# Kernel optimization log

Hardware: AMD Instinct MI355X
Metric: run time of the kernel (lower is better)

Reference implementation:

```python
import jax, jax.numpy as jnp
import numpy as np

EPS = 1e-12  # torch F.normalize eps

def _l2norm(v, axis):
    n = jnp.sqrt(jnp.sum(v * v, axis=axis, keepdims=True))
    return v / jnp.maximum(n, EPS)

def setup_inputs() -> dict:
    key = jax.random.key(0)
    k1, k2 = jax.random.split(key)
    B, N, D, K = 8, 2048, 128, 64
    x = jax.random.normal(k1, (B, N, D), dtype=jnp.float32)
    std1 = 1.0 / np.sqrt(K * D)
    centroids = jax.random.uniform(k2, (K, D), dtype=jnp.float32, minval=-std1, maxval=std1)
    return {"x": x, "centroids": centroids}

def reference(x, centroids):
    # x: [B, N, D], centroids: [K, D]
    B, N, D = x.shape
    K = centroids.shape[0]
    xn = _l2norm(x, axis=-1)                       # descriptor-wise L2 normalize
    res = xn[:, :, None, :] - centroids[None, None]  # [B, N, K, D]
    dist = jnp.sum(res * res, axis=-1)             # [B, N, K] squared distances
    assign = jax.nn.softmax(dist, axis=-1)         # softmax over clusters (NOTE: positive distances, as in source)
    vlad = jnp.einsum('bnk,bnkd->bkd', assign, res)  # weighted residual sum over N
    vlad = _l2norm(vlad, axis=2)                   # intra-normalization per cluster
    vlad = vlad.reshape(B, K * D)
    vlad = _l2norm(vlad, axis=1)                   # global L2 normalize
    return vlad
```

## Files before the change

kernel.cpp:

```cpp
#include <hip/hip_runtime.h>
#include <math.h>

#define BB 8
#define NN 2048
#define DD 128
#define KK 64
#define PP 64
#define NPB (NN / PP)
#define TI 16

__global__ __launch_bounds__(512)
__attribute__((amdgpu_waves_per_eu(4, 4)))
void netvlad_k1(
    const float* __restrict__ x, const float* __restrict__ cent,
    float* __restrict__ part_acc)
{
    const int b    = blockIdx.x >> 6;
    const int p    = blockIdx.x & 63;
    const int t    = threadIdx.x;
    const int h    = t >> 8;
    const int u    = t & 255;
    const int kq   = u >> 3;
    const int pr   = u & 7;
    const int dbase = pr * 16;
    const int wv   = u >> 6;

    __shared__ __align__(16) float xs[2][TI][DD];
    __shared__ __align__(16) float sL[2][TI][4];
    __shared__ __align__(16) float comb[256][36];
    __shared__ float sAc[32][2];

    int off[4];
    #pragma unroll
    for (int jj = 0; jj < 4; ++jj) off[jj] = dbase + (((jj + pr) & 3) << 2);

    const int i0 = u >> 4, tl = u & 15;
    const float* xr = x + ((size_t)b * NN + (size_t)p * NPB + h * TI + i0) * DD;
    float4 v0 = *(const float4*)(xr + tl * 4);
    float4 v1 = *(const float4*)(xr + 64 + tl * 4);

    float4 cA[4], cB[4];
    float cn2a = 0.f, cn2b = 0.f;
    #pragma unroll
    for (int jj = 0; jj < 4; ++jj) {
        cA[jj] = *(const float4*)(cent + (2 * kq) * DD + off[jj]);
        cB[jj] = *(const float4*)(cent + (2 * kq + 1) * DD + off[jj]);
        cn2a += cA[jj].x*cA[jj].x + cA[jj].y*cA[jj].y + cA[jj].z*cA[jj].z + cA[jj].w*cA[jj].w;
        cn2b += cB[jj].x*cB[jj].x + cB[jj].y*cB[jj].y + cB[jj].z*cB[jj].z + cB[jj].w*cB[jj].w;
    }
    #pragma unroll
    for (int m = 1; m < 8; m <<= 1) {
        cn2a += __shfl_xor(cn2a, m);
        cn2b += __shfl_xor(cn2b, m);
    }

    {
        float ss = v0.x*v0.x + v0.y*v0.y + v0.z*v0.z + v0.w*v0.w
                 + v1.x*v1.x + v1.y*v1.y + v1.z*v1.z + v1.w*v1.w;
        #pragma unroll
        for (int m = 1; m < 16; m <<= 1) ss += __shfl_xor(ss, m);
        const float rn = 1.0f / fmaxf(sqrtf(ss), 1e-12f);
        v0.x *= rn; v0.y *= rn; v0.z *= rn; v0.w *= rn;
        v1.x *= rn; v1.y *= rn; v1.z *= rn; v1.w *= rn;
        *(float4*)(&xs[h][i0][tl * 4])      = v0;
        *(float4*)(&xs[h][i0][64 + tl * 4]) = v1;
    }
    __syncthreads();

    float e0[TI], e1[TI];
    #pragma unroll
    for (int i = 0; i < TI; ++i) {
        float S0 = 0.f, S1 = 0.f;
        #pragma unroll
        for (int jj = 0; jj < 4; ++jj) {
            float4 v = *(const float4*)(&xs[h][i][off[jj]]);
            S0 += v.x*cA[jj].x + v.y*cA[jj].y + v.z*cA[jj].z + v.w*cA[jj].w;
            S1 += v.x*cB[jj].x + v.y*cB[jj].y + v.z*cB[jj].z + v.w*cB[jj].w;
        }
        #pragma unroll
        for (int m = 1; m < 8; m <<= 1) {
            S0 += __shfl_xor(S0, m);
            S1 += __shfl_xor(S1, m);
        }
        e0[i] = __expf(cn2a - 2.f * S0);
        e1[i] = __expf(cn2b - 2.f * S1);
        float es = e0[i] + e1[i];
        #pragma unroll
        for (int m = 8; m < 64; m <<= 1) es += __shfl_xor(es, m);
        if ((u & 63) == 0) sL[h][i][wv] = es;
    }
    __syncthreads();

    float4 acc0[4], acc1[4];
    #pragma unroll
    for (int jj = 0; jj < 4; ++jj) {
        acc0[jj] = make_float4(0.f, 0.f, 0.f, 0.f);
        acc1[jj] = make_float4(0.f, 0.f, 0.f, 0.f);
    }
    float sA0 = 0.f, sA1 = 0.f;
    #pragma unroll
    for (int i = 0; i < TI; ++i) {
        const float4 s4 = *(const float4*)(&sL[h][i][0]);
        const float rs = 1.0f / (s4.x + s4.y + s4.z + s4.w);
        const float a0 = e0[i] * rs, a1 = e1[i] * rs;
        sA0 += a0; sA1 += a1;
        #pragma unroll
        for (int jj = 0; jj < 4; ++jj) {
            float4 v = *(const float4*)(&xs[h][i][off[jj]]);
            acc0[jj].x += a0*v.x; acc0[jj].y += a0*v.y; acc0[jj].z += a0*v.z; acc0[jj].w += a0*v.w;
            acc1[jj].x += a1*v.x; acc1[jj].y += a1*v.y; acc1[jj].z += a1*v.z; acc1[jj].w += a1*v.w;
        }
    }

    if (h == 0) {
        #pragma unroll
        for (int jj = 0; jj < 4; ++jj) {
            *(float4*)(&comb[u][jj * 4])      = acc0[jj];
            *(float4*)(&comb[u][16 + jj * 4]) = acc1[jj];
        }
        if (pr == 0) { sAc[kq][0] = sA0; sAc[kq][1] = sA1; }
    }
    __syncthreads();

    if (h == 1) {
        sA0 += sAc[kq][0];
        sA1 += sAc[kq][1];
        const size_t base = (size_t)(b * PP + p) * KK * DD;
        #pragma unroll
        for (int jj = 0; jj < 4; ++jj) {
            const float4 c0 = *(const float4*)(cent + (2 * kq) * DD + off[jj]);
            const float4 c1 = *(const float4*)(cent + (2 * kq + 1) * DD + off[jj]);
            const float4 o0 = *(const float4*)(&comb[u][jj * 4]);
            const float4 o1 = *(const float4*)(&comb[u][16 + jj * 4]);
            float4 r0 = acc0[jj], r1 = acc1[jj];
            r0.x += o0.x; r0.y += o0.y; r0.z += o0.z; r0.w += o0.w;
            r1.x += o1.x; r1.y += o1.y; r1.z += o1.z; r1.w += o1.w;
            r0.x -= sA0 * c0.x; r0.y -= sA0 * c0.y;
            r0.z -= sA0 * c0.z; r0.w -= sA0 * c0.w;
            r1.x -= sA1 * c1.x; r1.y -= sA1 * c1.y;
            r1.z -= sA1 * c1.z; r1.w -= sA1 * c1.w;
            *(float4*)(part_acc + base + (2 * kq) * DD + off[jj])     = r0;
            *(float4*)(part_acc + base + (2 * kq + 1) * DD + off[jj]) = r1;
        }
    }
}

__global__ __launch_bounds__(512) void netvlad_k2(
    const float* __restrict__ part_acc, float* __restrict__ out)
{
    const int b  = blockIdx.x >> 6;
    const int k  = blockIdx.x & 63;
    const int t  = threadIdx.x;
    const int d4 = t & 31;
    const int ps = t >> 5;

    float4 acc = make_float4(0.f, 0.f, 0.f, 0.f);
    const float* base = part_acc + ((size_t)(b * PP) * KK + k) * DD + d4 * 4;
    #pragma unroll
    for (int j = 0; j < 4; ++j) {
        const float4 v = *(const float4*)(base + (size_t)(j * 16 + ps) * KK * DD);
        acc.x += v.x; acc.y += v.y; acc.z += v.z; acc.w += v.w;
    }

    __shared__ __align__(16) float4 red[16][32];
    red[ps][d4] = acc;
    __syncthreads();

    if (t < 32) {
        float4 v = red[0][t];
        #pragma unroll
        for (int s = 1; s < 16; ++s) {
            v.x += red[s][t].x; v.y += red[s][t].y;
            v.z += red[s][t].z; v.w += red[s][t].w;
        }
        float ss = v.x*v.x + v.y*v.y + v.z*v.z + v.w*v.w;
        #pragma unroll
        for (int m = 1; m < 32; m <<= 1) ss += __shfl_xor(ss, m);
        const float rn = 0.125f / fmaxf(sqrtf(ss), 1e-12f);
        v.x *= rn; v.y *= rn; v.z *= rn; v.w *= rn;
        *(float4*)(out + ((size_t)b * KK + k) * DD + t * 4) = v;
    }
}

extern "C" void kernel_launch(void* const* d_in, const int* in_sizes, int n_in,
                              void* d_out, int out_size, void* d_ws, size_t ws_size,
                              hipStream_t stream) {
    const float* x    = (const float*)d_in[0];
    const float* cent = (const float*)d_in[1];
    float* out = (float*)d_out;

    float* part_acc = (float*)d_ws;

    netvlad_k1<<<dim3(BB * PP), dim3(512), 0, stream>>>(x, cent, part_acc);
    netvlad_k2<<<dim3(BB * KK), dim3(512), 0, stream>>>(part_acc, out);
}
```

Baseline: 87.47 us.

## Replace per-block partial buffers with global atomic accumulation into VLAD

The first kernel no longer writes one partial VLAD per (batch, block) slab. Each block now atomically adds its residual sums into a single zeroed B×K×D buffer, so the second kernel only has to normalize rows instead of reducing 64 partials. This cuts workspace traffic from about 16 MB of writes and reads to a small buffer, and it adds a memset plus scalar float atomics with 64-way contention per address. Summation order also becomes nondeterministic.

```diff
diff --git a/kernel.cpp b/kernel.cpp
--- a/kernel.cpp
+++ b/kernel.cpp
@@ -13,7 +13,7 @@
 __attribute__((amdgpu_waves_per_eu(4, 4)))
 void netvlad_k1(
     const float* __restrict__ x, const float* __restrict__ cent,
-    float* __restrict__ part_acc)
+    float* __restrict__ vlad)
 {
     const int b    = blockIdx.x >> 6;
     const int p    = blockIdx.x & 63;
@@ -125,7 +125,6 @@
     if (h == 1) {
         sA0 += sAc[kq][0];
         sA1 += sAc[kq][1];
-        const size_t base = (size_t)(b * PP + p) * KK * DD;
         #pragma unroll
         for (int jj = 0; jj < 4; ++jj) {
             const float4 c0 = *(const float4*)(cent + (2 * kq) * DD + off[jj]);
@@ -139,40 +138,25 @@
             r0.z -= sA0 * c0.z; r0.w -= sA0 * c0.w;
             r1.x -= sA1 * c1.x; r1.y -= sA1 * c1.y;
             r1.z -= sA1 * c1.z; r1.w -= sA1 * c1.w;
-            *(float4*)(part_acc + base + (2 * kq) * DD + off[jj])     = r0;
-            *(float4*)(part_acc + base + (2 * kq + 1) * DD + off[jj]) = r1;
+            float* p0 = vlad + ((size_t)(b * KK) + 2 * kq)     * DD + off[jj];
+            float* p1 = vlad + ((size_t)(b * KK) + 2 * kq + 1) * DD + off[jj];
+            atomicAdd(p0 + 0, r0.x); atomicAdd(p0 + 1, r0.y);
+            atomicAdd(p0 + 2, r0.z); atomicAdd(p0 + 3, r0.w);
+            atomicAdd(p1 + 0, r1.x); atomicAdd(p1 + 1, r1.y);
+            atomicAdd(p1 + 2, r1.z); atomicAdd(p1 + 3, r1.w);
         }
     }
 }
 
-__global__ __launch_bounds__(512) void netvlad_k2(
-    const float* __restrict__ part_acc, float* __restrict__ out)
+__global__ __launch_bounds__(64) void netvlad_k2(
+    const float* __restrict__ vlad, float* __restrict__ out)
 {
-    const int b  = blockIdx.x >> 6;
-    const int k  = blockIdx.x & 63;
-    const int t  = threadIdx.x;
-    const int d4 = t & 31;
-    const int ps = t >> 5;
-
-    float4 acc = make_float4(0.f, 0.f, 0.f, 0.f);
-    const float* base = part_acc + ((size_t)(b * PP) * KK + k) * DD + d4 * 4;
-    #pragma unroll
-    for (int j = 0; j < 4; ++j) {
-        const float4 v = *(const float4*)(base + (size_t)(j * 16 + ps) * KK * DD);
-        acc.x += v.x; acc.y += v.y; acc.z += v.z; acc.w += v.w;
-    }
-
-    __shared__ __align__(16) float4 red[16][32];
-    red[ps][d4] = acc;
-    __syncthreads();
-
+    const int b = blockIdx.x >> 6;
+    const int k = blockIdx.x & 63;
+    const int t = threadIdx.x;
     if (t < 32) {
-        float4 v = red[0][t];
-        #pragma unroll
-        for (int s = 1; s < 16; ++s) {
-            v.x += red[s][t].x; v.y += red[s][t].y;
-            v.z += red[s][t].z; v.w += red[s][t].w;
-        }
+        const float4 v0 = *(const float4*)(vlad + ((size_t)(b * KK) + k) * DD + t * 4);
+        float4 v = v0;
         float ss = v.x*v.x + v.y*v.y + v.z*v.z + v.w*v.w;
         #pragma unroll
         for (int m = 1; m < 32; m <<= 1) ss += __shfl_xor(ss, m);
@@ -189,8 +173,9 @@
     const float* cent = (const float*)d_in[1];
     float* out = (float*)d_out;
 
-    float* part_acc = (float*)d_ws;
+    float* vlad = (float*)d_ws;
 
-    netvlad_k1<<<dim3(BB * PP), dim3(512), 0, stream>>>(x, cent, part_acc);
-    netvlad_k2<<<dim3(BB * KK), dim3(512), 0, stream>>>(part_acc, out);
+    hipMemsetAsync(d_ws, 0, (size_t)BB * KK * DD * 4, stream);
+    netvlad_k1<<<dim3(BB * PP), dim3(512), 0, stream>>>(x, cent, vlad);
+    netvlad_k2<<<dim3(BB * KK), dim3(64), 0, stream>>>(vlad, out);
 }
```

After: 280.4 us. 3.21x slower.
